# Optimization experiments

Hardware: AMD Instinct MI355X
Metric: run time of the kernel (lower is better)

Reference implementation:

```python
import jax, jax.numpy as jnp
import numpy as np

WIN = 7
SHIFT = 3
HEADS = 4
DIM = 128


def _rel_pos_index(wh, ww):
    coords = np.stack(np.meshgrid(np.arange(wh), np.arange(ww), indexing='ij')).reshape(2, -1)
    rel = (coords[:, :, None] - coords[:, None, :]).transpose(1, 2, 0)  # (N,N,2)
    rel[..., 0] += wh - 1
    rel[..., 1] += ww - 1
    rel[..., 0] *= 2 * ww - 1
    return rel.sum(-1)  # (N,N) int


def _shift_mask(H, W, wh, ww, sh, sw):
    img = np.zeros((H, W), dtype=np.float32)
    cnt = 0
    for hs in (slice(0, -wh), slice(-wh, -sh), slice(-sh, None)):
        for ws in (slice(0, -ww), slice(-ww, -sw), slice(-sw, None)):
            img[hs, ws] = cnt
            cnt += 1
    mw = img.reshape(H // wh, wh, W // ww, ww).transpose(0, 2, 1, 3).reshape(-1, wh * ww)
    diff = mw[:, :, None] - mw[:, None, :]
    return np.where(diff != 0, -100.0, 0.0).astype(np.float32)  # (nW,N,N)


def setup_inputs() -> dict:
    key = jax.random.key(0)
    ks = jax.random.split(key, 5)
    x = jax.random.normal(ks[0], (16, 112, 112, DIM), dtype=jnp.float32)
    w_qkv = jax.random.normal(ks[1], (DIM, 3 * DIM), dtype=jnp.float32) * 0.02
    b_qkv = jnp.zeros((3 * DIM,), dtype=jnp.float32)
    w_proj = jax.random.normal(ks[2], (DIM, DIM), dtype=jnp.float32) * 0.02
    b_proj = jnp.zeros((DIM,), dtype=jnp.float32)
    log_sigma = jnp.zeros((HEADS,), dtype=jnp.float32)  # sigma=1.0
    bias_table = jax.random.normal(ks[3], ((2 * WIN - 1) ** 2, HEADS), dtype=jnp.float32) * 0.02
    return {"x": x, "w_qkv": w_qkv, "b_qkv": b_qkv, "w_proj": w_proj,
            "b_proj": b_proj, "log_sigma": log_sigma, "bias_table": bias_table}


def reference(x, w_qkv, b_qkv, w_proj, b_proj, log_sigma, bias_table):
    B, H, W, C = x.shape
    wh = ww = WIN
    sh = sw = SHIFT
    heads = HEADS
    hd = C // heads
    N = wh * ww
    nWh, nWw = H // wh, W // ww

    shifted = jnp.roll(x, (-sh, -sw), axis=(1, 2))
    qkv = shifted @ w_qkv + b_qkv  # (B,H,W,3C)
    # window partition: -> (B*nW, 3, heads, N, hd)
    qkv = qkv.reshape(B, nWh, wh, nWw, ww, 3, heads, hd)
    qkv = qkv.transpose(0, 1, 3, 5, 6, 2, 4, 7).reshape(B * nWh * nWw, 3, heads, N, hd)
    q, k, v = qkv[:, 0], qkv[:, 1], qkv[:, 2]

    scale = hd ** -0.5
    q = q * scale
    k = k * scale
    q_sq = jnp.sum(q * q, -1, keepdims=True)               # (B_,h,N,1)
    k_sq = jnp.sum(k * k, -1, keepdims=True).swapaxes(-2, -1)  # (B_,h,1,N)
    qk = jnp.einsum('bhnd,bhmd->bhnm', q, k)
    dist_sq = jnp.maximum(q_sq + k_sq - 2.0 * qk, 1e-12)
    sigma_sq = jnp.exp(2.0 * log_sigma).reshape(1, heads, 1, 1)
    attn = (-0.5 / sigma_sq) * dist_sq                     # (B_,h,N,N)

    rpi = jnp.asarray(_rel_pos_index(wh, ww))
    bias = bias_table[rpi.reshape(-1)].reshape(N, N, heads).transpose(2, 0, 1)
    attn = attn + bias[None]

    mask = jnp.asarray(_shift_mask(H, W, wh, ww, sh, sw))  # (nW,N,N)
    attn = attn.reshape(B, nWh * nWw, heads, N, N) + mask[None, :, None]
    attn = jax.nn.softmax(attn, axis=-1).reshape(-1, heads, N, N)

    out = jnp.einsum('bhnm,bhmd->bhnd', attn, v)           # (B_,h,N,hd)
    out = out.transpose(0, 2, 1, 3).reshape(B, nWh, nWw, wh, ww, C)
    out = out.transpose(0, 1, 3, 2, 4, 5).reshape(B, H, W, C)
    out = jnp.roll(out, (sh, sw), axis=(1, 2))
    return out @ w_proj + b_proj
```

## Files before the change

### kernel.cpp

```cpp
#include <hip/hip_runtime.h>
#include <math.h>

#define IMG 112
#define CDIM 128
#define NTOK 49

__global__ __launch_bounds__(256, 4) void qkv_gemm_kernel(
    const float* __restrict__ x, const float* __restrict__ w,
    const float* __restrict__ bqkv, float* __restrict__ qkv)
{
    __shared__ float At[32][132];
    __shared__ float Bs[32][132];
    const int tid = threadIdx.x;
    const int m0 = blockIdx.x << 7;
    const int j0 = blockIdx.y << 7;
    const int tm = tid >> 4, tn = tid & 15;
    const float fscale = (j0 < 256) ? 0.17677669529663687f : 1.0f;

    float acc[8][8];
#pragma unroll
    for (int i = 0; i < 8; i++)
#pragma unroll
        for (int j = 0; j < 8; j++) acc[i][j] = 0.0f;

    for (int kc = 0; kc < 4; kc++) {
        if (kc) __syncthreads();
#pragma unroll
        for (int i = 0; i < 4; i++) {
            int idx = tid + (i << 8);
            int r = idx >> 3;
            int c4 = (idx & 7) << 2;
            int m = m0 + r;
            int b = m / (IMG * IMG);
            int rem = m - b * (IMG * IMG);
            int hh = rem / IMG;
            int ww_ = rem - hh * IMG;
            int hs = hh + 3; if (hs >= IMG) hs -= IMG;
            int ws = ww_ + 3; if (ws >= IMG) ws -= IMG;
            float4 v = *(const float4*)(x + ((size_t)((b * IMG + hs) * IMG + ws)) * CDIM + (kc << 5) + c4);
            At[c4 + 0][r] = v.x;
            At[c4 + 1][r] = v.y;
            At[c4 + 2][r] = v.z;
            At[c4 + 3][r] = v.w;
        }
#pragma unroll
        for (int i = 0; i < 4; i++) {
            int idx = tid + (i << 8);
            int c = idx >> 5;
            int j4 = (idx & 31) << 2;
            *(float4*)(&Bs[c][j4]) = *(const float4*)(w + (size_t)((kc << 5) + c) * 384 + j0 + j4);
        }
        __syncthreads();
#pragma unroll
        for (int c = 0; c < 32; c++) {
            float4 a0 = *(const float4*)(&At[c][tm << 3]);
            float4 a1 = *(const float4*)(&At[c][(tm << 3) + 4]);
            float4 b0 = *(const float4*)(&Bs[c][tn << 3]);
            float4 b1 = *(const float4*)(&Bs[c][(tn << 3) + 4]);
            float av[8] = {a0.x, a0.y, a0.z, a0.w, a1.x, a1.y, a1.z, a1.w};
            float bv[8] = {b0.x, b0.y, b0.z, b0.w, b1.x, b1.y, b1.z, b1.w};
#pragma unroll
            for (int ii = 0; ii < 8; ii++)
#pragma unroll
                for (int jj = 0; jj < 8; jj++) acc[ii][jj] = fmaf(av[ii], bv[jj], acc[ii][jj]);
        }
    }
    const int jb = j0 + (tn << 3);
    float4 bq0 = *(const float4*)(bqkv + jb);
    float4 bq1 = *(const float4*)(bqkv + jb + 4);
#pragma unroll
    for (int ii = 0; ii < 8; ii++) {
        size_t m = (size_t)(m0 + (tm << 3) + ii);
        float4 o0, o1;
        o0.x = (acc[ii][0] + bq0.x) * fscale;
        o0.y = (acc[ii][1] + bq0.y) * fscale;
        o0.z = (acc[ii][2] + bq0.z) * fscale;
        o0.w = (acc[ii][3] + bq0.w) * fscale;
        o1.x = (acc[ii][4] + bq1.x) * fscale;
        o1.y = (acc[ii][5] + bq1.y) * fscale;
        o1.z = (acc[ii][6] + bq1.z) * fscale;
        o1.w = (acc[ii][7] + bq1.w) * fscale;
        *(float4*)(qkv + m * 384 + jb) = o0;
        *(float4*)(qkv + m * 384 + jb + 4) = o1;
    }
}

#define KVSLAB 3136
#define OFF_OSB 12544
#define OFF_BT  18816
#define OFF_KSQ 19492
#define SM_FLOATS 19688

__global__ __launch_bounds__(256) void attn_kernel(
    const float* __restrict__ qkv, const float* __restrict__ wproj,
    const float* __restrict__ bproj, const float* __restrict__ lsig,
    const float* __restrict__ btab, float* __restrict__ out)
{
    __shared__ float sm[SM_FLOATS];
    const int tid = threadIdx.x;
    const int lane = tid & 63;
    const int h = tid >> 6;
    const int bx = blockIdx.x;
    const int b  = bx >> 8;
    const int wi = (bx >> 4) & 15;
    const int wj = bx & 15;

    float* kh  = sm + h * KVSLAB;
    float* vh  = kh + 1568;
    float* osb = sm + OFF_OSB;
    float* bts = sm + OFF_BT;
    float* ksq = sm + OFF_KSQ + h * 49;

    for (int i = tid; i < 676; i += 256) bts[i] = btab[i];

    const bool fi = (wi == 15), fj = (wj == 15);
    float4 q[8];
    float qsq = 0.0f;
    int cn = 0, rbase = 0;

    if (lane < NTOK) {
        int nh_ = lane / 7, nw_ = lane - (lane / 7) * 7;
        rbase = (nh_ * 13 + nw_) * 4 + h;
        cn = (fi ? (nh_ < 4 ? 1 : 2) : 0) * 3 + (fj ? (nw_ < 4 ? 1 : 2) : 0);
        size_t gm = (size_t)((b * IMG + wi * 7 + nh_) * IMG + wj * 7 + nw_);
        const float* rowp = qkv + gm * 384 + h * 32;
        float ks = 0.0f;
#pragma unroll
        for (int d4 = 0; d4 < 8; d4++) {
            float4 qv = *(const float4*)(rowp + (d4 << 2));
            q[d4] = qv;
            qsq = fmaf(qv.x, qv.x, qsq); qsq = fmaf(qv.y, qv.y, qsq);
            qsq = fmaf(qv.z, qv.z, qsq); qsq = fmaf(qv.w, qv.w, qsq);
            float4 kv = *(const float4*)(rowp + 128 + (d4 << 2));
            ks = fmaf(kv.x, kv.x, ks); ks = fmaf(kv.y, kv.y, ks);
            ks = fmaf(kv.z, kv.z, ks); ks = fmaf(kv.w, kv.w, ks);
            *(float4*)(kh + lane * 32 + ((d4 ^ (lane & 7)) << 2)) = kv;
            float4 vv = *(const float4*)(rowp + 256 + (d4 << 2));
            *(float4*)(vh + lane * 32 + ((d4 ^ (lane & 7)) << 2)) = vv;
        }
        ksq[lane] = ks;
    }
    __syncthreads();

    if (lane < NTOK) {
        const float coef = -0.5f * __expf(-2.0f * lsig[h]);
        float s[49];
#pragma unroll
        for (int m = 0; m < 49; m++) {
            const int mh = m / 7, mw = m - (m / 7) * 7;
            float qk = 0.0f;
#pragma unroll
            for (int d4 = 0; d4 < 8; d4++) {
                float4 k4 = *(const float4*)(kh + m * 32 + ((d4 ^ (m & 7)) << 2));
                qk = fmaf(q[d4].x, k4.x, qk); qk = fmaf(q[d4].y, k4.y, qk);
                qk = fmaf(q[d4].z, k4.z, qk); qk = fmaf(q[d4].w, k4.w, qk);
            }
            float dist = fmaxf(qsq + ksq[m] - 2.0f * qk, 1e-12f);
            float bias = bts[rbase + ((6 - mh) * 13 + (6 - mw)) * 4];
            int cm = (fi ? (mh < 4 ? 1 : 2) : 0) * 3 + (fj ? (mw < 4 ? 1 : 2) : 0);
            s[m] = fmaf(coef, dist, (cn != cm) ? bias - 100.0f : bias);
        }
        float mx = s[0];
#pragma unroll
        for (int m = 1; m < 49; m++) mx = fmaxf(mx, s[m]);
        float sum = 0.0f;
#pragma unroll
        for (int m = 0; m < 49; m++) { float e = __expf(s[m] - mx); s[m] = e; sum += e; }
        const float inv = 1.0f / sum;
        float4 o[8];
#pragma unroll
        for (int d4 = 0; d4 < 8; d4++) { o[d4].x = 0.f; o[d4].y = 0.f; o[d4].z = 0.f; o[d4].w = 0.f; }
#pragma unroll
        for (int m = 0; m < 49; m++) {
            const float p = s[m];
#pragma unroll
            for (int d4 = 0; d4 < 8; d4++) {
                float4 v4 = *(const float4*)(vh + m * 32 + ((d4 ^ (m & 7)) << 2));
                o[d4].x = fmaf(p, v4.x, o[d4].x);
                o[d4].y = fmaf(p, v4.y, o[d4].y);
                o[d4].z = fmaf(p, v4.z, o[d4].z);
                o[d4].w = fmaf(p, v4.w, o[d4].w);
            }
        }
#pragma unroll
        for (int d4 = 0; d4 < 8; d4++) {
            float4 ov;
            ov.x = o[d4].x * inv; ov.y = o[d4].y * inv;
            ov.z = o[d4].z * inv; ov.w = o[d4].w * inv;
            int gg = (h << 3) + d4;
            *(float4*)(osb + lane * 128 + ((gg ^ (lane & 7)) << 2)) = ov;
        }
    }
    __syncthreads();

    const int e4 = tid & 31;
    const int rowbase = tid >> 5;
    float4 bv = *(const float4*)(bproj + (e4 << 2));
    float4 pacc[7];
#pragma unroll
    for (int r = 0; r < 7; r++) pacc[r] = bv;

    float* wp = sm;
    for (int ch = 0; ch < 2; ch++) {
        __syncthreads();
        for (int i = tid; i < 2048; i += 256)
            ((float4*)wp)[i] = ((const float4*)(wproj + (ch << 13)))[i];
        __syncthreads();
#pragma unroll 4
        for (int c4 = 0; c4 < 16; c4++) {
            const int cb = c4 << 2;
            float4 w0 = *(const float4*)(wp + (cb + 0) * 128 + (e4 << 2));
            float4 w1 = *(const float4*)(wp + (cb + 1) * 128 + (e4 << 2));
            float4 w2 = *(const float4*)(wp + (cb + 2) * 128 + (e4 << 2));
            float4 w3 = *(const float4*)(wp + (cb + 3) * 128 + (e4 << 2));
            const int gg = (ch << 4) + c4;
#pragma unroll
            for (int r = 0; r < 7; r++) {
                int nn = rowbase + (r << 3);
                if (nn < NTOK) {
                    float4 o4 = *(const float4*)(osb + nn * 128 + ((gg ^ (nn & 7)) << 2));
                    float4 a = pacc[r];
                    a.x = fmaf(o4.x, w0.x, a.x); a.y = fmaf(o4.x, w0.y, a.y);
                    a.z = fmaf(o4.x, w0.z, a.z); a.w = fmaf(o4.x, w0.w, a.w);
                    a.x = fmaf(o4.y, w1.x, a.x); a.y = fmaf(o4.y, w1.y, a.y);
                    a.z = fmaf(o4.y, w1.z, a.z); a.w = fmaf(o4.y, w1.w, a.w);
                    a.x = fmaf(o4.z, w2.x, a.x); a.y = fmaf(o4.z, w2.y, a.y);
                    a.z = fmaf(o4.z, w2.z, a.z); a.w = fmaf(o4.z, w2.w, a.w);
                    a.x = fmaf(o4.w, w3.x, a.x); a.y = fmaf(o4.w, w3.y, a.y);
                    a.z = fmaf(o4.w, w3.z, a.z); a.w = fmaf(o4.w, w3.w, a.w);
                    pacc[r] = a;
                }
            }
        }
    }
#pragma unroll
    for (int r = 0; r < 7; r++) {
        int nn = rowbase + (r << 3);
        if (nn < NTOK) {
            int ph = nn / 7, pw = nn - (nn / 7) * 7;
            int ho = wi * 7 + ph + 3; if (ho >= IMG) ho -= IMG;
            int wo = wj * 7 + pw + 3; if (wo >= IMG) wo -= IMG;
            *(float4*)(out + ((size_t)((b * IMG + ho) * IMG + wo)) * CDIM + (e4 << 2)) = pacc[r];
        }
    }
}

extern "C" void kernel_launch(void* const* d_in, const int* in_sizes, int n_in,
                              void* d_out, int out_size, void* d_ws, size_t ws_size,
                              hipStream_t stream)
{
    const float* x         = (const float*)d_in[0];
    const float* w_qkv     = (const float*)d_in[1];
    const float* b_qkv     = (const float*)d_in[2];
    const float* w_proj    = (const float*)d_in[3];
    const float* b_proj    = (const float*)d_in[4];
    const float* log_sigma = (const float*)d_in[5];
    const float* bias_tab  = (const float*)d_in[6];
    float* out = (float*)d_out;
    float* qkv = (float*)d_ws;

    dim3 g1(200704 / 128, 3);
    qkv_gemm_kernel<<<g1, 256, 0, stream>>>(x, w_qkv, b_qkv, qkv);
    attn_kernel<<<4096, 256, 0, stream>>>(qkv, w_proj, b_proj, log_sigma, bias_tab, out);
}
```

Before: 737.0 us.

## Store QKV window-major, shrink attention LDS, and shuffle k-norms

The QKV GEMM epilogue now writes rows in window-partitioned order, so each attention block reads one contiguous 49x384 slab instead of scattered image rows. The GEMM fragment mapping changes to strided 4-wide halves to reduce LDS bank conflicts. The attention kernel reuses the K/V LDS region for the output staging and the projection weights, loaded in four smaller chunks. This cuts shared memory enough to target three blocks per CU, and k-norms move to wave shuffles with a simplified mask computation. The price is an extra barrier, more chunk syncs, and per-row index divisions in the GEMM epilogue.

```diff
diff --git a/kernel.cpp b/kernel.cpp
--- a/kernel.cpp
+++ b/kernel.cpp
@@ -53,10 +53,10 @@
         __syncthreads();
 #pragma unroll
         for (int c = 0; c < 32; c++) {
-            float4 a0 = *(const float4*)(&At[c][tm << 3]);
-            float4 a1 = *(const float4*)(&At[c][(tm << 3) + 4]);
-            float4 b0 = *(const float4*)(&Bs[c][tn << 3]);
-            float4 b1 = *(const float4*)(&Bs[c][(tn << 3) + 4]);
+            float4 a0 = *(const float4*)(&At[c][tm << 2]);
+            float4 a1 = *(const float4*)(&At[c][64 + (tm << 2)]);
+            float4 b0 = *(const float4*)(&Bs[c][tn << 2]);
+            float4 b1 = *(const float4*)(&Bs[c][64 + (tn << 2)]);
             float av[8] = {a0.x, a0.y, a0.z, a0.w, a1.x, a1.y, a1.z, a1.w};
             float bv[8] = {b0.x, b0.y, b0.z, b0.w, b1.x, b1.y, b1.z, b1.w};
 #pragma unroll
@@ -65,33 +65,43 @@
                 for (int jj = 0; jj < 8; jj++) acc[ii][jj] = fmaf(av[ii], bv[jj], acc[ii][jj]);
         }
     }
-    const int jb = j0 + (tn << 3);
-    float4 bq0 = *(const float4*)(bqkv + jb);
-    float4 bq1 = *(const float4*)(bqkv + jb + 4);
-#pragma unroll
-    for (int ii = 0; ii < 8; ii++) {
-        size_t m = (size_t)(m0 + (tm << 3) + ii);
-        float4 o0, o1;
-        o0.x = (acc[ii][0] + bq0.x) * fscale;
-        o0.y = (acc[ii][1] + bq0.y) * fscale;
-        o0.z = (acc[ii][2] + bq0.z) * fscale;
-        o0.w = (acc[ii][3] + bq0.w) * fscale;
-        o1.x = (acc[ii][4] + bq1.x) * fscale;
-        o1.y = (acc[ii][5] + bq1.y) * fscale;
-        o1.z = (acc[ii][6] + bq1.z) * fscale;
-        o1.w = (acc[ii][7] + bq1.w) * fscale;
-        *(float4*)(qkv + m * 384 + jb) = o0;
-        *(float4*)(qkv + m * 384 + jb + 4) = o1;
+    const int jb0 = j0 + (tn << 2);
+    float4 bq0 = *(const float4*)(bqkv + jb0);
+    float4 bq1 = *(const float4*)(bqkv + jb0 + 64);
+#pragma unroll
+    for (int ih = 0; ih < 2; ih++) {
+#pragma unroll
+        for (int ii = 0; ii < 4; ii++) {
+            int r = (ih << 6) + (tm << 2) + ii;
+            int m = m0 + r;
+            int b = m / (IMG * IMG);
+            int rem = m - b * (IMG * IMG);
+            int hh = rem / IMG;
+            int ww_ = rem - hh * IMG;
+            int wi = hh / 7, ph = hh - wi * 7;
+            int wj = ww_ / 7, pw = ww_ - wj * 7;
+            size_t mp = (size_t)(((b * 16 + wi) * 16 + wj) * 49 + ph * 7 + pw);
+            int ai = (ih << 2) + ii;
+            float4 o0, o1;
+            o0.x = (acc[ai][0] + bq0.x) * fscale;
+            o0.y = (acc[ai][1] + bq0.y) * fscale;
+            o0.z = (acc[ai][2] + bq0.z) * fscale;
+            o0.w = (acc[ai][3] + bq0.w) * fscale;
+            o1.x = (acc[ai][4] + bq1.x) * fscale;
+            o1.y = (acc[ai][5] + bq1.y) * fscale;
+            o1.z = (acc[ai][6] + bq1.z) * fscale;
+            o1.w = (acc[ai][7] + bq1.w) * fscale;
+            *(float4*)(qkv + mp * 384 + jb0) = o0;
+            *(float4*)(qkv + mp * 384 + jb0 + 64) = o1;
+        }
     }
 }
 
 #define KVSLAB 3136
-#define OFF_OSB 12544
-#define OFF_BT  18816
-#define OFF_KSQ 19492
-#define SM_FLOATS 19688
-
-__global__ __launch_bounds__(256) void attn_kernel(
+#define OFF_BT 12544
+#define SM_FLOATS 13220
+
+__global__ __launch_bounds__(256, 3) void attn_kernel(
     const float* __restrict__ qkv, const float* __restrict__ wproj,
     const float* __restrict__ bproj, const float* __restrict__ lsig,
     const float* __restrict__ btab, float* __restrict__ out)
@@ -101,30 +111,30 @@
     const int lane = tid & 63;
     const int h = tid >> 6;
     const int bx = blockIdx.x;
-    const int b  = bx >> 8;
     const int wi = (bx >> 4) & 15;
     const int wj = bx & 15;
 
     float* kh  = sm + h * KVSLAB;
     float* vh  = kh + 1568;
-    float* osb = sm + OFF_OSB;
     float* bts = sm + OFF_BT;
-    float* ksq = sm + OFF_KSQ + h * 49;
+    float* osb = sm;
+    float* wp  = sm + 6272;
 
     for (int i = tid; i < 676; i += 256) bts[i] = btab[i];
 
     const bool fi = (wi == 15), fj = (wj == 15);
     float4 q[8];
-    float qsq = 0.0f;
-    int cn = 0, rbase = 0;
+    float qsq = 0.0f, ks = 0.0f;
+    int pbit = 0, qbit = 0, rbase = 0;
+
+    const float* blkbase = qkv + (size_t)bx * (49 * 384);
 
     if (lane < NTOK) {
         int nh_ = lane / 7, nw_ = lane - (lane / 7) * 7;
         rbase = (nh_ * 13 + nw_) * 4 + h;
-        cn = (fi ? (nh_ < 4 ? 1 : 2) : 0) * 3 + (fj ? (nw_ < 4 ? 1 : 2) : 0);
-        size_t gm = (size_t)((b * IMG + wi * 7 + nh_) * IMG + wj * 7 + nw_);
-        const float* rowp = qkv + gm * 384 + h * 32;
-        float ks = 0.0f;
+        pbit = (nh_ < 4) ? 1 : 0;
+        qbit = (nw_ < 4) ? 1 : 0;
+        const float* rowp = blkbase + lane * 384 + h * 32;
 #pragma unroll
         for (int d4 = 0; d4 < 8; d4++) {
             float4 qv = *(const float4*)(rowp + (d4 << 2));
@@ -138,9 +148,13 @@
             float4 vv = *(const float4*)(rowp + 256 + (d4 << 2));
             *(float4*)(vh + lane * 32 + ((d4 ^ (lane & 7)) << 2)) = vv;
         }
-        ksq[lane] = ks;
     }
     __syncthreads();
+
+    float4 o[8];
+#pragma unroll
+    for (int d4 = 0; d4 < 8; d4++) { o[d4].x = 0.f; o[d4].y = 0.f; o[d4].z = 0.f; o[d4].w = 0.f; }
+    float inv = 0.0f;
 
     if (lane < NTOK) {
         const float coef = -0.5f * __expf(-2.0f * lsig[h]);
@@ -155,10 +169,11 @@
                 qk = fmaf(q[d4].x, k4.x, qk); qk = fmaf(q[d4].y, k4.y, qk);
                 qk = fmaf(q[d4].z, k4.z, qk); qk = fmaf(q[d4].w, k4.w, qk);
             }
-            float dist = fmaxf(qsq + ksq[m] - 2.0f * qk, 1e-12f);
+            float ksm = __shfl(ks, m, 64);
+            float dist = fmaxf(qsq + ksm - 2.0f * qk, 1e-12f);
             float bias = bts[rbase + ((6 - mh) * 13 + (6 - mw)) * 4];
-            int cm = (fi ? (mh < 4 ? 1 : 2) : 0) * 3 + (fj ? (mw < 4 ? 1 : 2) : 0);
-            s[m] = fmaf(coef, dist, (cn != cm) ? bias - 100.0f : bias);
+            int msk = (fi ? (pbit ^ ((mh < 4) ? 1 : 0)) : 0) | (fj ? (qbit ^ ((mw < 4) ? 1 : 0)) : 0);
+            s[m] = fmaf(coef, dist, msk ? bias - 100.0f : bias);
         }
         float mx = s[0];
 #pragma unroll
@@ -166,10 +181,7 @@
         float sum = 0.0f;
 #pragma unroll
         for (int m = 0; m < 49; m++) { float e = __expf(s[m] - mx); s[m] = e; sum += e; }
-        const float inv = 1.0f / sum;
-        float4 o[8];
-#pragma unroll
-        for (int d4 = 0; d4 < 8; d4++) { o[d4].x = 0.f; o[d4].y = 0.f; o[d4].z = 0.f; o[d4].w = 0.f; }
+        inv = 1.0f / sum;
 #pragma unroll
         for (int m = 0; m < 49; m++) {
             const float p = s[m];
@@ -182,6 +194,10 @@
                 o[d4].w = fmaf(p, v4.w, o[d4].w);
             }
         }
+    }
+    __syncthreads();
+
+    if (lane < NTOK) {
 #pragma unroll
         for (int d4 = 0; d4 < 8; d4++) {
             float4 ov;
@@ -191,6 +207,8 @@
             *(float4*)(osb + lane * 128 + ((gg ^ (lane & 7)) << 2)) = ov;
         }
     }
+    for (int i = tid; i < 1024; i += 256)
+        ((float4*)wp)[i] = ((const float4*)wproj)[i];
     __syncthreads();
 
     const int e4 = tid & 31;
@@ -200,20 +218,15 @@
 #pragma unroll
     for (int r = 0; r < 7; r++) pacc[r] = bv;
 
-    float* wp = sm;
-    for (int ch = 0; ch < 2; ch++) {
-        __syncthreads();
-        for (int i = tid; i < 2048; i += 256)
-            ((float4*)wp)[i] = ((const float4*)(wproj + (ch << 13)))[i];
-        __syncthreads();
+    for (int ch = 0; ch < 4; ch++) {
 #pragma unroll 4
-        for (int c4 = 0; c4 < 16; c4++) {
+        for (int c4 = 0; c4 < 8; c4++) {
             const int cb = c4 << 2;
             float4 w0 = *(const float4*)(wp + (cb + 0) * 128 + (e4 << 2));
             float4 w1 = *(const float4*)(wp + (cb + 1) * 128 + (e4 << 2));
             float4 w2 = *(const float4*)(wp + (cb + 2) * 128 + (e4 << 2));
             float4 w3 = *(const float4*)(wp + (cb + 3) * 128 + (e4 << 2));
-            const int gg = (ch << 4) + c4;
+            const int gg = (ch << 3) + c4;
 #pragma unroll
             for (int r = 0; r < 7; r++) {
                 int nn = rowbase + (r << 3);
@@ -232,7 +245,14 @@
                 }
             }
         }
-    }
+        if (ch < 3) {
+            __syncthreads();
+            for (int i = tid; i < 1024; i += 256)
+                ((float4*)wp)[i] = ((const float4*)(wproj + ((ch + 1) << 12)))[i];
+            __syncthreads();
+        }
+    }
+    const int b = bx >> 8;
 #pragma unroll
     for (int r = 0; r < 7; r++) {
         int nn = rowbase + (r << 3);
```

Result: faster. 708.6 us (-3.9%).
